# Kernel optimization log

Hardware: AMD Instinct MI355X
Metric: run time of the kernel (lower is better)

The kernel has to match this reference:

```python
import jax, jax.numpy as jnp
import numpy as np

B, N, START = 16, 16, 2048
D, H, HK, DH, CTX = 4096, 32, 8, 128, 4096
T = START + N
REP = H // HK
ROPE_THETA = 500000.0


def setup_inputs() -> dict:
    key = jax.random.key(0)
    ks = jax.random.split(key, 8)
    x = jax.random.normal(ks[0], (B, N, D), jnp.float32)
    # rotary frequencies for absolute positions START..T-1
    half = DH // 2
    inv_freq = 1.0 / (ROPE_THETA ** (np.arange(half, dtype=np.float64) * 2.0 / DH))
    pos = np.arange(START, T, dtype=np.float64)
    ang = pos[:, None] * inv_freq[None, :]  # (N, DH//2)
    freqs_cos = jnp.asarray(np.cos(ang), jnp.float32)
    freqs_sin = jnp.asarray(np.sin(ang), jnp.float32)
    # causal additive mask: query i (abs pos START+i) may attend to key j <= START+i
    i = np.arange(N)[:, None]
    j = np.arange(T)[None, :]
    mask = np.where(j <= START + i, 0.0, -1e9).astype(np.float32)
    mask = jnp.asarray(mask)[None, None]  # (1,1,N,T)
    cache_k = jax.random.normal(ks[1], (B, HK, CTX, DH), jnp.float32)
    cache_v = jax.random.normal(ks[2], (B, HK, CTX, DH), jnp.float32)
    s = 0.02
    wq = jax.random.normal(ks[3], (D, H * DH), jnp.float32) * s
    wk = jax.random.normal(ks[4], (D, HK * DH), jnp.float32) * s
    wv = jax.random.normal(ks[5], (D, HK * DH), jnp.float32) * s
    wo = jax.random.normal(ks[6], (D, D), jnp.float32) * s
    return {"x": x, "freqs_cos": freqs_cos, "freqs_sin": freqs_sin, "mask": mask,
            "cache_k": cache_k, "cache_v": cache_v,
            "wq": wq, "wk": wk, "wv": wv, "wo": wo, "start_pos": START}


def _rope(t, cos, sin):
    # t: (B, N, h, DH); cos/sin: (N, DH//2) -> broadcast (1, N, 1, DH//2)
    tr = t.reshape(*t.shape[:-1], -1, 2)
    a, b = tr[..., 0], tr[..., 1]
    c = cos[None, :, None, :]
    s = sin[None, :, None, :]
    out = jnp.stack([a * c - b * s, a * s + b * c], axis=-1)
    return out.reshape(t.shape)


def reference(x, freqs_cos, freqs_sin, mask, cache_k, cache_v, wq, wk, wv, wo, start_pos):
    Bx, Nx, _ = x.shape
    t_end = start_pos + Nx
    xq = (x @ wq).reshape(Bx, Nx, H, DH)
    xk = (x @ wk).reshape(Bx, Nx, HK, DH)
    xv = (x @ wv).reshape(Bx, Nx, HK, DH)
    xq = _rope(xq, freqs_cos, freqs_sin)
    xk = _rope(xk, freqs_cos, freqs_sin)
    xq = xq.transpose(0, 2, 1, 3)  # (B,H,N,DH)
    xk = xk.transpose(0, 2, 1, 3)  # (B,HK,N,DH)
    xv = xv.transpose(0, 2, 1, 3)
    # KV-cache scatter update, then slice to current length
    cache_k = cache_k.at[:, :, start_pos:t_end].set(xk)
    cache_v = cache_v.at[:, :, start_pos:t_end].set(xv)
    k = cache_k[:, :, :t_end]  # (B,HK,T,DH)
    v = cache_v[:, :, :t_end]
    # GQA masked SDPA
    q = xq.reshape(Bx, HK, REP, Nx, DH)
    scale = 1.0 / jnp.sqrt(jnp.float32(DH))
    scores = jnp.einsum('bkrnd,bktd->bkrnt', q, k) * scale
    scores = scores + mask[:, :, None]  # (1,1,1,N,T) broadcast
    p = jax.nn.softmax(scores, axis=-1)
    z = jnp.einsum('bkrnt,bktd->bkrnd', p, v)
    z = z.reshape(Bx, H, Nx, DH).transpose(0, 2, 1, 3).reshape(Bx, Nx, D)
    return z @ wo
```

## Files before the change

### kernel.cpp

```cpp
#include <hip/hip_runtime.h>


#define CTX 4096

typedef __attribute__((ext_vector_type(8))) short short8;
typedef __attribute__((ext_vector_type(4))) float f32x4;

__device__ __forceinline__ unsigned short f2bf(float f) {
  union { float f; unsigned u; } a; a.f = f;
  unsigned r = a.u + 0x7FFFu + ((a.u >> 16) & 1u);
  return (unsigned short)(r >> 16);
}

__device__ __forceinline__ f32x4 mfma_bf16(short8 a, short8 b, f32x4 c) {
  return __builtin_amdgcn_mfma_f32_16x16x32_bf16(a, b, c, 0, 0, 0);
}

__device__ __forceinline__ void gll16(const unsigned short* g, unsigned short* l) {
  __builtin_amdgcn_global_load_lds(
      (__attribute__((address_space(1))) unsigned int*)(g),
      (__attribute__((address_space(3))) unsigned int*)(l), 16, 0, 0);
}

__global__ __launch_bounds__(256) void k_prep(const float* __restrict__ wq,
    const float* __restrict__ wk, const float* __restrict__ wv,
    const float* __restrict__ wo, const float* __restrict__ x,
    unsigned short* __restrict__ wqkvT, unsigned short* __restrict__ woT,
    unsigned short* __restrict__ xb)
{
  const int bid = blockIdx.x, tid = threadIdx.x;
  if (bid >= 10240) {
    int e4 = (bid - 10240) * 256 + tid;
    float4 v = ((const float4*)x)[e4];
    ushort4 o; o.x = f2bf(v.x); o.y = f2bf(v.y); o.z = f2bf(v.z); o.w = f2bf(v.w);
    ((ushort4*)xb)[e4] = o;
    return;
  }
  __shared__ unsigned short Ts[64][66];
  const float* src; unsigned short* dst; int N; int t = bid;
  if (t < 4096)      {            src = wq; dst = wqkvT;                        N = 4096; }
  else if (t < 5120) { t -= 4096; src = wk; dst = wqkvT + (size_t)4096 * 4096;  N = 1024; }
  else if (t < 6144) { t -= 5120; src = wv; dst = wqkvT + (size_t)5120 * 4096;  N = 1024; }
  else               { t -= 6144; src = wo; dst = woT;                          N = 4096; }
  const int kt = t & 63, bn = t >> 6;
  const int k0 = kt * 64, n0 = bn * 64;
#pragma unroll
  for (int i = 0; i < 4; ++i) {
    int u = tid + i * 256;
    int k = u >> 4, n4 = u & 15;
    float4 v = *(const float4*)(src + (size_t)(k0 + k) * N + n0 + n4 * 4);
    Ts[k][n4 * 4 + 0] = f2bf(v.x); Ts[k][n4 * 4 + 1] = f2bf(v.y);
    Ts[k][n4 * 4 + 2] = f2bf(v.z); Ts[k][n4 * 4 + 3] = f2bf(v.w);
  }
  __syncthreads();
#pragma unroll
  for (int i = 0; i < 2; ++i) {
    int u = tid + i * 256;
    int nn = u >> 3, cc = u & 7;
    unsigned short v[8];
#pragma unroll
    for (int j = 0; j < 8; ++j) v[j] = Ts[cc * 8 + j][nn];
    *(short8*)(dst + (size_t)(n0 + nn) * 4096 + k0 + cc * 8) = *(const short8*)v;
  }
}

__global__ __launch_bounds__(256) void k_gemm(const unsigned short* __restrict__ A,
    const unsigned short* __restrict__ BT, float* __restrict__ Cp, int Ntot)
{
  __shared__ unsigned short sA[128 * 64];
  __shared__ unsigned short sB[64 * 64];
  const int tid = threadIdx.x;
  const int w = tid >> 6, lane = tid & 63, quad = lane >> 4, l16 = lane & 15;
  const int wm = (w & 1) << 6, wn = (w >> 1) << 5;
  const int bn = blockIdx.x, bm = blockIdx.y, ks = blockIdx.z;
  const int r8 = lane >> 3, c8 = (lane & 7) << 3;

  const unsigned short* Ab = A + (size_t)(bm * 128) * 4096 + (ks << 11);
  const unsigned short* Bb = BT + (size_t)(bn * 64) * 4096 + (ks << 11);

  f32x4 acc[4][2];
#pragma unroll
  for (int mf = 0; mf < 4; ++mf)
#pragma unroll
    for (int nf = 0; nf < 2; ++nf) acc[mf][nf] = (f32x4){0.f, 0.f, 0.f, 0.f};

  for (int kt = 0; kt < 32; ++kt) {
#pragma unroll
    for (int i = 0; i < 4; ++i)
      gll16(Ab + (size_t)(w * 32 + i * 8 + r8) * 4096 + kt * 64 + c8,
            &sA[(w * 32 + i * 8) * 64]);
#pragma unroll
    for (int i = 0; i < 2; ++i)
      gll16(Bb + (size_t)(w * 16 + i * 8 + r8) * 4096 + kt * 64 + c8,
            &sB[(w * 16 + i * 8) * 64]);
    __syncthreads();
#pragma unroll
    for (int kk = 0; kk < 2; ++kk) {
      short8 af[4], bfr[2];
#pragma unroll
      for (int mf = 0; mf < 4; ++mf)
        af[mf] = *(const short8*)&sA[(wm + mf * 16 + l16) * 64 + kk * 32 + quad * 8];
#pragma unroll
      for (int nf = 0; nf < 2; ++nf)
        bfr[nf] = *(const short8*)&sB[(wn + nf * 16 + l16) * 64 + kk * 32 + quad * 8];
#pragma unroll
      for (int mf = 0; mf < 4; ++mf)
#pragma unroll
        for (int nf = 0; nf < 2; ++nf)
          acc[mf][nf] = mfma_bf16(af[mf], bfr[nf], acc[mf][nf]);
    }
    __syncthreads();
  }

  float* Cz = Cp + (size_t)ks * 256 * Ntot;
#pragma unroll
  for (int mf = 0; mf < 4; ++mf)
#pragma unroll
    for (int nf = 0; nf < 2; ++nf)
#pragma unroll
      for (int r = 0; r < 4; ++r)
        Cz[(size_t)(bm * 128 + wm + mf * 16 + quad * 4 + r) * Ntot
           + bn * 64 + wn + nf * 16 + l16] = acc[mf][nf][r];
}

__global__ __launch_bounds__(256) void k_kvfin(const float* __restrict__ qp,
    const float* __restrict__ fcos, const float* __restrict__ fsin,
    float* __restrict__ ck, float* __restrict__ cv)
{
  const float* qp1 = qp + (size_t)256 * 6144;
  int id = blockIdx.x * 256 + threadIdx.x;
  if (id < 131072) {
    int m = id >> 9, pc = id & 511;
    int b = m >> 4, npos = m & 15;
    int hk = pc >> 6, fi = pc & 63;
    size_t off = (size_t)m * 6144 + 4096 + hk * 128 + 2 * fi;
    float a  = qp[off] + qp1[off];
    float b2 = qp[off + 1] + qp1[off + 1];
    float c = fcos[npos * 64 + fi], s = fsin[npos * 64 + fi];
    float* dst = ck + ((size_t)(b * 8 + hk) * CTX + 2048 + npos) * 128 + 2 * fi;
    dst[0] = a * c - b2 * s;
    dst[1] = a * s + b2 * c;
  } else {
    int e = id - 131072;
    int m = e >> 10, cc = e & 1023;
    int b = m >> 4, npos = m & 15;
    int hk = cc >> 7, dh = cc & 127;
    size_t off = (size_t)m * 6144 + 5120 + cc;
    cv[((size_t)(b * 8 + hk) * CTX + 2048 + npos) * 128 + dh] = qp[off] + qp1[off];
  }
}

__global__ __launch_bounds__(256) void k_attn(const float* __restrict__ qp,
    const float* __restrict__ ck, const float* __restrict__ cv,
    const float* __restrict__ fcos, const float* __restrict__ fsin,
    float* __restrict__ zpO, float* __restrict__ zpL)
{
  __shared__ unsigned short Ks[32][136];
  __shared__ unsigned short Vs[128][40];
  __shared__ unsigned short Ps[4][16][40];

  const int tid = threadIdx.x;
  const int w = tid >> 6, lane = tid & 63, quad = lane >> 4, l16 = lane & 15;
  const int bid = blockIdx.x;
  const int split = bid & 3, hk = (bid >> 2) & 7, b = bid >> 5;
  const int h = hk * 4 + w;
  const float scale = 0.08838834764831845f;

  short8 qf[4];
  {
    const float* q0 = qp + (size_t)(b * 16 + l16) * 6144 + h * 128;
    const float* q1 = q0 + (size_t)256 * 6144;
#pragma unroll
    for (int kf = 0; kf < 4; ++kf) {
      float t[8];
#pragma unroll
      for (int j = 0; j < 4; ++j) {
        int o = kf * 32 + quad * 8 + j;
        t[j]     = q0[o] + q1[o];
        t[4 + j] = q0[o + 4] + q1[o + 4];
      }
#pragma unroll
      for (int p = 0; p < 4; ++p) {
        int dh = kf * 32 + quad * 8 + 2 * p;
        int fi = dh >> 1;
        float c = fcos[l16 * 64 + fi], s = fsin[l16 * 64 + fi];
        float a = t[2 * p], b2 = t[2 * p + 1];
        qf[kf][2 * p]     = (short)f2bf((a * c - b2 * s) * scale);
        qf[kf][2 * p + 1] = (short)f2bf((a * s + b2 * c) * scale);
      }
    }
  }

  const float* Kg = ck + (size_t)(b * 8 + hk) * CTX * 128;
  const float* Vg = cv + (size_t)(b * 8 + hk) * CTX * 128;
  const int tb = split * 512;
  const int NT = (split == 3) ? 17 : 16;

  f32x4 O[8];
#pragma unroll
  for (int df = 0; df < 8; ++df) O[df] = (f32x4){0.f, 0.f, 0.f, 0.f};
  float lp[4] = {0.f, 0.f, 0.f, 0.f};

  float4 pk[4], pv[4];
#define A_LOAD(IT_) do { \
    _Pragma("unroll") for (int i = 0; i < 4; ++i) { \
      int u = tid + (i << 8); int trow = u >> 5, c4 = u & 31; \
      size_t off = (size_t)(tb + (IT_) * 32 + trow) * 128 + c4 * 4; \
      pk[i] = *(const float4*)(Kg + off); \
      pv[i] = *(const float4*)(Vg + off); \
    } } while (0)
#define A_STORE() do { \
    _Pragma("unroll") for (int i = 0; i < 4; ++i) { \
      int u = tid + (i << 8); int trow = u >> 5, c4 = u & 31; \
      ushort4 k4; k4.x = f2bf(pk[i].x); k4.y = f2bf(pk[i].y); \
      k4.z = f2bf(pk[i].z); k4.w = f2bf(pk[i].w); \
      *(ushort4*)&Ks[trow][c4 * 4] = k4; \
      Vs[c4 * 4 + 0][trow] = f2bf(pv[i].x); \
      Vs[c4 * 4 + 1][trow] = f2bf(pv[i].y); \
      Vs[c4 * 4 + 2][trow] = f2bf(pv[i].z); \
      Vs[c4 * 4 + 3][trow] = f2bf(pv[i].w); \
    } } while (0)

  A_LOAD(0);
  A_STORE();
  __syncthreads();

  for (int it = 0; it < NT; ++it) {
    if (it + 1 < NT) A_LOAD(it + 1);

    f32x4 S0 = (f32x4){0.f,0.f,0.f,0.f}, S1 = (f32x4){0.f,0.f,0.f,0.f};
#pragma unroll
    for (int kf = 0; kf < 4; ++kf) {
      short8 k0 = *(const short8*)&Ks[l16][kf * 32 + quad * 8];
      short8 k1 = *(const short8*)&Ks[16 + l16][kf * 32 + quad * 8];
      S0 = mfma_bf16(qf[kf], k0, S0);
      S1 = mfma_bf16(qf[kf], k1, S1);
    }

    const bool lastT = (split == 3) && (it == 16);
    float p0[4], p1[4];
#pragma unroll
    for (int r = 0; r < 4; ++r) {
      int row = quad * 4 + r;
      if (!lastT) { p0[r] = __expf(S0[r]); p1[r] = __expf(S1[r]); }
      else        { p0[r] = (l16 <= row) ? __expf(S0[r]) : 0.f; p1[r] = 0.f; }
      lp[r] += p0[r] + p1[r];
      Ps[w][row][l16]      = f2bf(p0[r]);
      Ps[w][row][16 + l16] = f2bf(p1[r]);
    }

    short8 pf = *(const short8*)&Ps[w][l16][quad * 8];
#pragma unroll
    for (int df = 0; df < 8; ++df) {
      short8 vb = *(const short8*)&Vs[df * 16 + l16][quad * 8];
      O[df] = mfma_bf16(pf, vb, O[df]);
    }

    __syncthreads();
    if (it + 1 < NT) A_STORE();
    __syncthreads();
  }
#undef A_LOAD
#undef A_STORE

#pragma unroll
  for (int r = 0; r < 4; ++r)
#pragma unroll
    for (int off = 1; off < 16; off <<= 1) lp[r] += __shfl_xor(lp[r], off);

#pragma unroll
  for (int df = 0; df < 8; ++df)
#pragma unroll
    for (int r = 0; r < 4; ++r)
      zpO[(size_t)(split * 256 + b * 16 + quad * 4 + r) * 4096 + h * 128 + df * 16 + l16]
          = O[df][r];

  if (l16 == 0) {
#pragma unroll
    for (int r = 0; r < 4; ++r)
      zpL[((split * 16 + b) * 32 + h) * 16 + quad * 4 + r] = lp[r];
  }
}

__global__ __launch_bounds__(256) void k_combine(const float* __restrict__ zpO,
    const float* __restrict__ zpL, unsigned short* __restrict__ zb)
{
  int e = blockIdx.x * 256 + threadIdx.x;
  int m = e >> 12, col = e & 4095;
  int b = m >> 4, npos = m & 15, h = col >> 7;
  float num = 0.f, den = 0.f;
#pragma unroll
  for (int s = 0; s < 4; ++s) {
    num += zpO[(size_t)s * 1048576 + e];
    den += zpL[((s * 16 + b) * 32 + h) * 16 + npos];
  }
  zb[e] = f2bf(num / den);
}

__global__ __launch_bounds__(256) void k_fin(const float* __restrict__ op,
                                             float* __restrict__ out)
{
  int e4 = blockIdx.x * 256 + threadIdx.x;
  float4 a = ((const float4*)op)[e4];
  float4 b = ((const float4*)(op + (size_t)1048576))[e4];
  float4 o; o.x = a.x + b.x; o.y = a.y + b.y; o.z = a.z + b.z; o.w = a.w + b.w;
  ((float4*)out)[e4] = o;
}

extern "C" void kernel_launch(void* const* d_in, const int* in_sizes, int n_in,
                              void* d_out, int out_size, void* d_ws, size_t ws_size,
                              hipStream_t stream) {
  const float* x  = (const float*)d_in[0];
  const float* fc = (const float*)d_in[1];
  const float* fs = (const float*)d_in[2];
  float* ck = (float*)d_in[4];
  float* cv = (float*)d_in[5];
  const float* wq = (const float*)d_in[6];
  const float* wk = (const float*)d_in[7];
  const float* wv = (const float*)d_in[8];
  const float* wo = (const float*)d_in[9];
  float* out = (float*)d_out;

  char* ws = (char*)d_ws;
#define MB(x) ((size_t)(x) << 20)
  unsigned short* xb    = (unsigned short*)(ws);
  unsigned short* wqkvT = (unsigned short*)(ws + MB(2));
  unsigned short* woT   = (unsigned short*)(ws + MB(50));
  float*          qpart = (float*)(ws + MB(82));
  unsigned short* zb    = (unsigned short*)(ws + MB(95));
  float*          zpO   = (float*)(ws + MB(97));
  float*          zpL   = (float*)(ws + MB(113));
  float*          opart = (float*)(ws + MB(114));
#undef MB

  k_prep<<<11264, 256, 0, stream>>>(wq, wk, wv, wo, x, wqkvT, woT, xb);
  k_gemm<<<dim3(96, 2, 2), 256, 0, stream>>>(xb, wqkvT, qpart, 6144);
  k_kvfin<<<1536, 256, 0, stream>>>(qpart, fc, fs, ck, cv);
  k_attn<<<512, 256, 0, stream>>>(qpart, ck, cv, fc, fs, zpO, zpL);
  k_combine<<<4096, 256, 0, stream>>>(zpO, zpL, zb);
  k_gemm<<<dim3(64, 2, 2), 256, 0, stream>>>(zb, woT, opart, 4096);
  k_fin<<<1024, 256, 0, stream>>>(opart, out);
}
```

Before: 675.5 us.

## Split GEMM K four ways, precompute bf16 roped Q, store partial O in bf16

```diff
diff --git a/kernel.cpp b/kernel.cpp
--- a/kernel.cpp
+++ b/kernel.cpp
@@ -53,14 +53,14 @@
     Ts[k][n4 * 4 + 2] = f2bf(v.z); Ts[k][n4 * 4 + 3] = f2bf(v.w);
   }
   __syncthreads();
-#pragma unroll
-  for (int i = 0; i < 2; ++i) {
-    int u = tid + i * 256;
-    int nn = u >> 3, cc = u & 7;
-    unsigned short v[8];
-#pragma unroll
-    for (int j = 0; j < 8; ++j) v[j] = Ts[cc * 8 + j][nn];
-    *(short8*)(dst + (size_t)(n0 + nn) * 4096 + k0 + cc * 8) = *(const short8*)v;
+  {
+    int nn = tid >> 2, seg = tid & 3;
+    unsigned short v[16];
+#pragma unroll
+    for (int j = 0; j < 16; ++j) v[j] = Ts[seg * 16 + j][nn];
+    unsigned short* d = dst + (size_t)(n0 + nn) * 4096 + k0 + seg * 16;
+    *(short8*)d       = *(const short8*)&v[0];
+    *(short8*)(d + 8) = *(const short8*)&v[8];
   }
 }
 
@@ -75,8 +75,8 @@
   const int bn = blockIdx.x, bm = blockIdx.y, ks = blockIdx.z;
   const int r8 = lane >> 3, c8 = (lane & 7) << 3;
 
-  const unsigned short* Ab = A + (size_t)(bm * 128) * 4096 + (ks << 11);
-  const unsigned short* Bb = BT + (size_t)(bn * 64) * 4096 + (ks << 11);
+  const unsigned short* Ab = A + (size_t)(bm * 128) * 4096 + (ks << 10);
+  const unsigned short* Bb = BT + (size_t)(bn * 64) * 4096 + (ks << 10);
 
   f32x4 acc[4][2];
 #pragma unroll
@@ -84,7 +84,7 @@
 #pragma unroll
     for (int nf = 0; nf < 2; ++nf) acc[mf][nf] = (f32x4){0.f, 0.f, 0.f, 0.f};
 
-  for (int kt = 0; kt < 32; ++kt) {
+  for (int kt = 0; kt < 16; ++kt) {
 #pragma unroll
     for (int i = 0; i < 4; ++i)
       gll16(Ab + (size_t)(w * 32 + i * 8 + r8) * 4096 + kt * 64 + c8,
@@ -125,38 +125,55 @@
 
 __global__ __launch_bounds__(256) void k_kvfin(const float* __restrict__ qp,
     const float* __restrict__ fcos, const float* __restrict__ fsin,
-    float* __restrict__ ck, float* __restrict__ cv)
-{
-  const float* qp1 = qp + (size_t)256 * 6144;
+    float* __restrict__ ck, float* __restrict__ cv, unsigned short* __restrict__ qbf)
+{
+  const float scale = 0.08838834764831845f;
+  const size_t PS = (size_t)256 * 6144;
   int id = blockIdx.x * 256 + threadIdx.x;
-  if (id < 131072) {
-    int m = id >> 9, pc = id & 511;
+  if (id < 524288) {
+    int m = id >> 11, pc = id & 2047;
+    int h = pc >> 6, fi = pc & 63, npos = m & 15;
+    size_t off = (size_t)m * 6144 + h * 128 + 2 * fi;
+    float a = 0.f, b2 = 0.f;
+#pragma unroll
+    for (int s = 0; s < 4; ++s) { a += qp[s * PS + off]; b2 += qp[s * PS + off + 1]; }
+    float c = fcos[npos * 64 + fi], sn = fsin[npos * 64 + fi];
+    unsigned short o0 = f2bf((a * c - b2 * sn) * scale);
+    unsigned short o1 = f2bf((a * sn + b2 * c) * scale);
+    qbf[(size_t)m * 4096 + h * 128 + 2 * fi]     = o0;
+    qbf[(size_t)m * 4096 + h * 128 + 2 * fi + 1] = o1;
+  } else if (id < 655360) {
+    int e = id - 524288;
+    int m = e >> 9, pc = e & 511;
+    int hk = pc >> 6, fi = pc & 63;
     int b = m >> 4, npos = m & 15;
-    int hk = pc >> 6, fi = pc & 63;
     size_t off = (size_t)m * 6144 + 4096 + hk * 128 + 2 * fi;
-    float a  = qp[off] + qp1[off];
-    float b2 = qp[off + 1] + qp1[off + 1];
-    float c = fcos[npos * 64 + fi], s = fsin[npos * 64 + fi];
+    float a = 0.f, b2 = 0.f;
+#pragma unroll
+    for (int s = 0; s < 4; ++s) { a += qp[s * PS + off]; b2 += qp[s * PS + off + 1]; }
+    float c = fcos[npos * 64 + fi], sn = fsin[npos * 64 + fi];
     float* dst = ck + ((size_t)(b * 8 + hk) * CTX + 2048 + npos) * 128 + 2 * fi;
-    dst[0] = a * c - b2 * s;
-    dst[1] = a * s + b2 * c;
+    dst[0] = a * c - b2 * sn;
+    dst[1] = a * sn + b2 * c;
   } else {
-    int e = id - 131072;
+    int e = id - 655360;
     int m = e >> 10, cc = e & 1023;
     int b = m >> 4, npos = m & 15;
     int hk = cc >> 7, dh = cc & 127;
     size_t off = (size_t)m * 6144 + 5120 + cc;
-    cv[((size_t)(b * 8 + hk) * CTX + 2048 + npos) * 128 + dh] = qp[off] + qp1[off];
-  }
-}
-
-__global__ __launch_bounds__(256) void k_attn(const float* __restrict__ qp,
+    float a = 0.f;
+#pragma unroll
+    for (int s = 0; s < 4; ++s) a += qp[s * PS + off];
+    cv[((size_t)(b * 8 + hk) * CTX + 2048 + npos) * 128 + dh] = a;
+  }
+}
+
+__global__ __launch_bounds__(256) void k_attn(const unsigned short* __restrict__ qbf,
     const float* __restrict__ ck, const float* __restrict__ cv,
-    const float* __restrict__ fcos, const float* __restrict__ fsin,
-    float* __restrict__ zpO, float* __restrict__ zpL)
+    unsigned short* __restrict__ zpO, float* __restrict__ zpL)
 {
   __shared__ unsigned short Ks[32][136];
-  __shared__ unsigned short Vs[128][40];
+  __shared__ unsigned short Vs[128][34];
   __shared__ unsigned short Ps[4][16][40];
 
   const int tid = threadIdx.x;
@@ -164,31 +181,13 @@
   const int bid = blockIdx.x;
   const int split = bid & 3, hk = (bid >> 2) & 7, b = bid >> 5;
   const int h = hk * 4 + w;
-  const float scale = 0.08838834764831845f;
 
   short8 qf[4];
   {
-    const float* q0 = qp + (size_t)(b * 16 + l16) * 6144 + h * 128;
-    const float* q1 = q0 + (size_t)256 * 6144;
-#pragma unroll
-    for (int kf = 0; kf < 4; ++kf) {
-      float t[8];
-#pragma unroll
-      for (int j = 0; j < 4; ++j) {
-        int o = kf * 32 + quad * 8 + j;
-        t[j]     = q0[o] + q1[o];
-        t[4 + j] = q0[o + 4] + q1[o + 4];
-      }
-#pragma unroll
-      for (int p = 0; p < 4; ++p) {
-        int dh = kf * 32 + quad * 8 + 2 * p;
-        int fi = dh >> 1;
-        float c = fcos[l16 * 64 + fi], s = fsin[l16 * 64 + fi];
-        float a = t[2 * p], b2 = t[2 * p + 1];
-        qf[kf][2 * p]     = (short)f2bf((a * c - b2 * s) * scale);
-        qf[kf][2 * p + 1] = (short)f2bf((a * s + b2 * c) * scale);
-      }
-    }
+    const unsigned short* qrow = qbf + (size_t)(b * 16 + l16) * 4096 + h * 128;
+#pragma unroll
+    for (int kf = 0; kf < 4; ++kf)
+      qf[kf] = *(const short8*)(qrow + kf * 32 + quad * 8);
   }
 
   const float* Kg = ck + (size_t)(b * 8 + hk) * CTX * 128;
@@ -273,7 +272,7 @@
 #pragma unroll
     for (int r = 0; r < 4; ++r)
       zpO[(size_t)(split * 256 + b * 16 + quad * 4 + r) * 4096 + h * 128 + df * 16 + l16]
-          = O[df][r];
+          = f2bf(O[df][r]);
 
   if (l16 == 0) {
 #pragma unroll
@@ -282,7 +281,7 @@
   }
 }
 
-__global__ __launch_bounds__(256) void k_combine(const float* __restrict__ zpO,
+__global__ __launch_bounds__(256) void k_combine(const unsigned short* __restrict__ zpO,
     const float* __restrict__ zpL, unsigned short* __restrict__ zb)
 {
   int e = blockIdx.x * 256 + threadIdx.x;
@@ -291,7 +290,9 @@
   float num = 0.f, den = 0.f;
 #pragma unroll
   for (int s = 0; s < 4; ++s) {
-    num += zpO[(size_t)s * 1048576 + e];
+    union { unsigned u; float f; } cv2;
+    cv2.u = (unsigned)zpO[(size_t)s * 1048576 + e] << 16;
+    num += cv2.f;
     den += zpL[((s * 16 + b) * 32 + h) * 16 + npos];
   }
   zb[e] = f2bf(num / den);
@@ -301,9 +302,12 @@
                                              float* __restrict__ out)
 {
   int e4 = blockIdx.x * 256 + threadIdx.x;
-  float4 a = ((const float4*)op)[e4];
-  float4 b = ((const float4*)(op + (size_t)1048576))[e4];
-  float4 o; o.x = a.x + b.x; o.y = a.y + b.y; o.z = a.z + b.z; o.w = a.w + b.w;
+  float4 o = ((const float4*)op)[e4];
+#pragma unroll
+  for (int s = 1; s < 4; ++s) {
+    float4 p = ((const float4*)(op + (size_t)s * 1048576))[e4];
+    o.x += p.x; o.y += p.y; o.z += p.z; o.w += p.w;
+  }
   ((float4*)out)[e4] = o;
 }
 
@@ -327,17 +331,18 @@
   unsigned short* wqkvT = (unsigned short*)(ws + MB(2));
   unsigned short* woT   = (unsigned short*)(ws + MB(50));
   float*          qpart = (float*)(ws + MB(82));
-  unsigned short* zb    = (unsigned short*)(ws + MB(95));
-  float*          zpO   = (float*)(ws + MB(97));
-  float*          zpL   = (float*)(ws + MB(113));
-  float*          opart = (float*)(ws + MB(114));
+  unsigned short* zb    = (unsigned short*)(ws + MB(108));
+  unsigned short* zpO   = (unsigned short*)(ws + MB(110));
+  float*          zpL   = (float*)(ws + MB(118));
+  float*          opart = (float*)(ws + MB(119));
+  unsigned short* qbf   = (unsigned short*)(ws + MB(136));
 #undef MB
 
   k_prep<<<11264, 256, 0, stream>>>(wq, wk, wv, wo, x, wqkvT, woT, xb);
-  k_gemm<<<dim3(96, 2, 2), 256, 0, stream>>>(xb, wqkvT, qpart, 6144);
-  k_kvfin<<<1536, 256, 0, stream>>>(qpart, fc, fs, ck, cv);
-  k_attn<<<512, 256, 0, stream>>>(qpart, ck, cv, fc, fs, zpO, zpL);
+  k_gemm<<<dim3(96, 2, 4), 256, 0, stream>>>(xb, wqkvT, qpart, 6144);
+  k_kvfin<<<3584, 256, 0, stream>>>(qpart, fc, fs, ck, cv, qbf);
+  k_attn<<<512, 256, 0, stream>>>(qbf, ck, cv, zpO, zpL);
   k_combine<<<4096, 256, 0, stream>>>(zpO, zpL, zb);
-  k_gemm<<<dim3(64, 2, 2), 256, 0, stream>>>(zb, woT, opart, 4096);
+  k_gemm<<<dim3(64, 2, 4), 256, 0, stream>>>(zb, woT, opart, 4096);
   k_fin<<<1024, 256, 0, stream>>>(opart, out);
 }
```

Measured after the change: 655.9 us. 2.9% less time.
